# Kernel optimization log

Measured on AMD Instinct MI355X. Metric: run time of the kernel, lower is better.

Reference implementation:

```python
import jax, jax.numpy as jnp
import numpy as np

B, N, M, D, H, DK = 4, 2048, 1024, 512, 8, 64  # H*DK == D (required by residual E + E_)
SCALE = 1.0 / np.sqrt(DK)
NEG = -9e15


def setup_inputs() -> dict:
    key = jax.random.key(0)
    ks = jax.random.split(key, 24)
    def W(k, din, dout):
        return (0.02 * jax.random.truncated_normal(k, -2.0, 2.0, (din, dout))).astype(jnp.float32)
    inp = {
        'X': jax.random.normal(ks[0], (B, N, D), jnp.float32),
        'incidence_matrix': jax.random.randint(ks[1], (B, N, M), 0, 2, jnp.int32),
        'attn_bias': jnp.zeros((1,), jnp.float32),
        'E': jax.random.normal(ks[2], (B, M, D), jnp.float32),
        'Wqn': W(ks[3], D, H * DK), 'bqn': jnp.zeros((H * DK,), jnp.float32),
        'Wkn': W(ks[4], D, H * DK), 'bkn': jnp.zeros((H * DK,), jnp.float32),
        'Wvn': W(ks[5], D, H * DK), 'bvn': jnp.zeros((H * DK,), jnp.float32),
        'Wqe': W(ks[6], D, H * DK), 'bqe': jnp.zeros((H * DK,), jnp.float32),
        'Wke': W(ks[7], D, H * DK), 'bke': jnp.zeros((H * DK,), jnp.float32),
        'Wve': W(ks[8], D, H * DK), 'bve': jnp.zeros((H * DK,), jnp.float32),
        'Wm1': W(ks[9], D, D), 'bm1': jnp.zeros((D,), jnp.float32),
        'Wm2': W(ks[10], D, D), 'bm2': jnp.zeros((D,), jnp.float32),
        'g_ln': jnp.ones((D,), jnp.float32), 'b_ln': jnp.zeros((D,), jnp.float32),
    }
    return inp


def _heads(x, Wt, b):
    # [B, L, D] -> [B, H, L, DK]
    b_, l_ = x.shape[0], x.shape[1]
    return (x @ Wt + b).reshape(b_, l_, H, DK).transpose(0, 2, 1, 3)


def _merge(x):
    # [B, H, L, DK] -> [B, L, H*DK]
    b_, _, l_, _ = x.shape
    return x.transpose(0, 2, 1, 3).reshape(b_, l_, H * DK)


def _layernorm(x, g, b, eps=1e-7):
    mu = jnp.mean(x, axis=-1, keepdims=True)
    var = jnp.var(x, axis=-1, keepdims=True)
    return (x - mu) * jax.lax.rsqrt(var + eps) * g + b


def _gelu(x):
    return jax.nn.gelu(x, approximate=False)


def reference(X, incidence_matrix, attn_bias, E,
              Wqn, bqn, Wkn, bkn, Wvn, bvn,
              Wqe, bqe, Wke, bke, Wve, bve,
              Wm1, bm1, Wm2, bm2, g_ln, b_ln):
    q_n = _heads(X, Wqn, bqn)   # [B,H,N,DK]
    k_n = _heads(X, Wkn, bkn)
    v_n = _heads(X, Wvn, bvn)
    q_e = _heads(E, Wqe, bqe)   # [B,H,M,DK]

    # edge attends over nodes: [B,H,M,N], masked by incidence^T
    att_e = jnp.einsum('bhmd,bhnd->bhmn', q_e, k_n) * SCALE
    mask_e = (incidence_matrix > 0).transpose(0, 2, 1)[:, None, :, :]  # [B,1,M,N]
    att_e = jnp.where(mask_e, att_e, NEG)
    w_e = jax.nn.softmax(att_e, axis=-1)
    E_ = _gelu(jnp.einsum('bhmn,bhnd->bhmd', w_e, v_n))
    E_ = _merge(E_)                                   # [B,M,D]
    E_ = _layernorm(E + E_, g_ln, b_ln)
    E_ = _gelu(E_ @ Wm1 + bm1) @ Wm2 + bm2            # MLP

    k_e = _heads(E_, Wke, bke)  # [B,H,M,DK]
    v_e = _heads(E_, Wve, bve)

    # node attends over edges: [B,H,N,M], masked by incidence
    att_n = jnp.einsum('bhnd,bhmd->bhnm', q_n, k_e) * SCALE
    mask_n = (incidence_matrix > 0)[:, None, :, :]    # [B,1,N,M]
    att_n = jnp.where(mask_n, att_n, NEG)
    w_n = jax.nn.softmax(att_n, axis=-1)
    X_ = _gelu(jnp.einsum('bhnm,bhmd->bhnd', w_n, v_e))
    X_ = _merge(X_)                                   # [B,N,D]
    return (X_, E_)
```

## Files before the change

### kernel.cpp

```cpp
#include <hip/hip_runtime.h>

typedef unsigned short u16;
typedef unsigned int   u32;
typedef unsigned long long u64;

typedef __attribute__((ext_vector_type(8))) short  bf16x8;
typedef __attribute__((ext_vector_type(16))) float f32x16;

#define SC2 0.1803368801111243f
#define CS2 11.541560327111707f

__device__ __forceinline__ float bf2f(u16 h) { return __uint_as_float(((u32)h) << 16); }
__device__ __forceinline__ u16 f2bf(float f) {
  u32 u = __float_as_uint(f);
  return (u16)((u + 0x7FFFu + ((u >> 16) & 1u)) >> 16);
}
__device__ __forceinline__ float gelu_f(float x) {
  return 0.5f * x * (1.0f + erff(x * 0.70710678118654752440f));
}
__device__ __forceinline__ void unpack8(uint4 u, float* d) {
  d[0] = __uint_as_float(u.x << 16); d[1] = __uint_as_float(u.x & 0xffff0000u);
  d[2] = __uint_as_float(u.y << 16); d[3] = __uint_as_float(u.y & 0xffff0000u);
  d[4] = __uint_as_float(u.z << 16); d[5] = __uint_as_float(u.z & 0xffff0000u);
  d[6] = __uint_as_float(u.w << 16); d[7] = __uint_as_float(u.w & 0xffff0000u);
}
__device__ __forceinline__ void dma16(const u16* g, u16* l) {
  __builtin_amdgcn_global_load_lds(
      (const __attribute__((address_space(1))) u32*)g,
      (__attribute__((address_space(3))) u32*)l, 16, 0, 0);
}

__global__ void detect_dtype(const u16* __restrict__ X, u32* __restrict__ flag) {
  int lane = threadIdx.x;
  int bad = 0;
  #pragma unroll
  for (int i = 0; i < 8; ++i) {
    u16 v = X[i * 64 + lane];
    int e = (v >> 7) & 0xFF;
    if (e >= 0x88) bad++;
  }
  #pragma unroll
  for (int o = 1; o < 64; o <<= 1) bad += __shfl_xor(bad, o);
  if (lane == 0) *flag = (bad > 16) ? 1u : 0u;
}

__global__ __launch_bounds__(256) void fill_diag(u32* __restrict__ out, float base,
                                                 const u32* __restrict__ flag) {
  float v = base + (*flag ? 4000.0f : 0.0f);
  u16 h = f2bf(v);
  out[blockIdx.x * 256 + threadIdx.x] = (u32)h | ((u32)h << 16);
}

__global__ __launch_bounds__(256) void conv_bf16(const void* __restrict__ src,
                                                 u16* __restrict__ dst, int n,
                                                 const u32* __restrict__ flag) {
  int i = (blockIdx.x * 256 + threadIdx.x) * 8;
  if (i >= n) return;
  if (*flag) {
    const float* s = (const float*)src + i;
    float4 a = *(const float4*)s;
    float4 b = *(const float4*)(s + 4);
    uint4 o;
    o.x = (u32)f2bf(a.x) | ((u32)f2bf(a.y) << 16);
    o.y = (u32)f2bf(a.z) | ((u32)f2bf(a.w) << 16);
    o.z = (u32)f2bf(b.x) | ((u32)f2bf(b.y) << 16);
    o.w = (u32)f2bf(b.z) | ((u32)f2bf(b.w) << 16);
    *(uint4*)(dst + i) = o;
  } else {
    *(uint4*)(dst + i) = *(const uint4*)((const u16*)src + i);
  }
}

__global__ __launch_bounds__(256) void conv_vec10(
    const void* p0, const void* p1, const void* p2, const void* p3, const void* p4,
    const void* p5, const void* p6, const void* p7, const void* p8, const void* p9,
    u16* __restrict__ dst, const u32* __restrict__ flag) {
  const void* ps[10] = {p0, p1, p2, p3, p4, p5, p6, p7, p8, p9};
  int fl = (int)(*flag);
  for (int idx = threadIdx.x; idx < 5120; idx += 256) {
    int slot = idx >> 9, off = idx & 511;
    u16 v;
    if (fl) v = f2bf(((const float*)ps[slot])[off]);
    else    v = ((const u16*)ps[slot])[off];
    dst[idx] = v;
  }
}

__global__ __launch_bounds__(256) void wtrans(
    const void* w0, const void* w1, const void* w2, const void* w3,
    const void* w4, const void* w5, const void* w6, const void* w7,
    u16* __restrict__ WT, const u32* __restrict__ flag) {
  const void* wsrc[8] = {w0, w1, w2, w3, w4, w5, w6, w7};
  __shared__ u16 tile[32][33];
  int z = blockIdx.z;
  const void* W = wsrc[z];
  u16* Wt = WT + (size_t)z * 262144;
  int fl = (int)(*flag);
  int tx = threadIdx.x & 31, ty = threadIdx.x >> 5;
  int bx = blockIdx.x * 32, by = blockIdx.y * 32;
  #pragma unroll
  for (int i = 0; i < 4; ++i) {
    int r = ty + 8 * i;
    size_t src = (size_t)(by + r) * 512 + bx + tx;
    tile[r][tx] = fl ? f2bf(((const float*)W)[src]) : ((const u16*)W)[src];
  }
  __syncthreads();
  #pragma unroll
  for (int i = 0; i < 4; ++i) {
    int r = ty + 8 * i;
    Wt[(size_t)(bx + r) * 512 + by + tx] = tile[tx][r];
  }
}

__global__ __launch_bounds__(256) void transposeV(const u16* __restrict__ Vp,
                                                  u16* __restrict__ VT, int Lk) {
  __shared__ u16 tile[64][72];
  int t = threadIdx.x;
  int nt = blockIdx.x;
  int bh = blockIdx.y;
  int nw = Lk >> 6;
  const u16* src = Vp + ((size_t)bh * Lk + nt * 64) * 64;
  int key = t >> 2, seg = t & 3;
  int dc0 = seg * 2, dc1 = seg * 2 + 1;
  uint4 a  = *(const uint4*)(src + key * 64 + ((dc0 ^ (key & 7)) << 3));
  uint4 b2 = *(const uint4*)(src + key * 64 + ((dc1 ^ (key & 7)) << 3));
  *(uint4*)&tile[key][dc0 * 8] = a;
  *(uint4*)&tile[key][dc1 * 8] = b2;
  __syncthreads();
  int d = t >> 2;
  u32 wb[8];
  #pragma unroll
  for (int i = 0; i < 8; ++i) {
    u32 lo = tile[seg * 16 + 2 * i][d];
    u32 hi = tile[seg * 16 + 2 * i + 1][d];
    wb[i] = lo | (hi << 16);
  }
  u16* base = VT + (((size_t)bh * nw + nt) * 64 + d) * 64;
  int kc0 = seg * 2, kc1 = seg * 2 + 1;
  uint4 o0; o0.x = wb[0]; o0.y = wb[1]; o0.z = wb[2]; o0.w = wb[3];
  uint4 o1; o1.x = wb[4]; o1.y = wb[5]; o1.z = wb[6]; o1.w = wb[7];
  *(uint4*)(base + ((kc0 ^ (d & 7)) << 3)) = o0;
  *(uint4*)(base + ((kc1 ^ (d & 7)) << 3)) = o1;
}

__global__ __launch_bounds__(256) void pack_rows(const int* __restrict__ inc,
                                                 u64* __restrict__ packNT) {
  int gid  = blockIdx.x * 4 + (threadIdx.x >> 6);
  int lane = threadIdx.x & 63;
  int w  = gid & 15;
  int bn = gid >> 4;
  int b = bn >> 11, n = bn & 2047;
  int v = inc[(size_t)bn * 1024 + (w << 6) + lane];
  u64 mask = __ballot(v > 0);
  if (lane == 0) packNT[((size_t)(b * 16 + w)) * 2048 + n] = mask;
}

__global__ __launch_bounds__(256) void pack_cols(const int* __restrict__ inc,
                                                 u64* __restrict__ packTT) {
  int m = blockIdx.x * 256 + threadIdx.x;
  int w = blockIdx.y;
  int b = blockIdx.z;
  const int* base = inc + ((size_t)b * 2048 + (size_t)w * 64) * 1024 + m;
  u64 out = 0;
  #pragma unroll 8
  for (int j = 0; j < 64; ++j)
    if (base[(size_t)j * 1024] > 0) out |= (1ull << j);
  packTT[((size_t)(b * 32 + w)) * 1024 + m] = out;
}

__global__ __launch_bounds__(256) void gemm_tiled(const u16* __restrict__ A,
                                                  const u16* __restrict__ Wt0, u32 wtStride,
                                                  const u16* __restrict__ bias0, u32 bStride,
                                                  u16* __restrict__ C0, u32 cStride,
                                                  int act, int blocksPerMat,
                                                  u32 modeMask, int lkshift,
                                                  void* __restrict__ out2, size_t out2_off,
                                                  const u32* __restrict__ flag) {
  __shared__ u16 As[2][8192];
  __shared__ u16 Bs[2][8192];
  int mat = blockIdx.x / blocksPerMat;
  int blk = blockIdx.x % blocksPerMat;
  const u16* Wt = Wt0 + (size_t)mat * wtStride;
  const u16* bias = bias0 + (size_t)mat * bStride;
  u16* C = C0 + (size_t)mat * cStride;
  int mode = (modeMask >> mat) & 1u;
  int f32o = out2 ? (int)(*flag) : 0;
  int tm = blk >> 2, tn = blk & 3;
  int m0 = tm * 128, n0 = tn * 128;

  int t = threadIdx.x;
  int wave = t >> 6, lane = t & 63;
  int nl = lane & 31, h32 = lane >> 5;
  int wm = wave >> 1, wn = wave & 1;

  int srow = lane >> 3;
  int gch  = (lane & 7) ^ srow;
  const u16* Ab = A  + ((size_t)m0 + wave * 32) * 512 + (size_t)srow * 512 + gch * 8;
  const u16* Bb = Wt + ((size_t)n0 + wave * 32) * 512 + (size_t)srow * 512 + gch * 8;
  u16* AsW = &As[0][0] + wave * 32 * 64;
  u16* BsW = &Bs[0][0] + wave * 32 * 64;

  #pragma unroll
  for (int c = 0; c < 4; ++c) {
    dma16(Ab + (size_t)c * 8 * 512, AsW + c * 8 * 64);
    dma16(Bb + (size_t)c * 8 * 512, BsW + c * 8 * 64);
  }
  __syncthreads();

  f32x16 a00 = {}, a01 = {}, a10 = {}, a11 = {};

  for (int kk = 0; kk < 8; ++kk) {
    int buf = kk & 1;
    if (kk + 1 < 8) {
      int k0n = (kk + 1) * 64;
      u16* AD = &As[buf ^ 1][0] + wave * 32 * 64;
      u16* BD = &Bs[buf ^ 1][0] + wave * 32 * 64;
      #pragma unroll
      for (int c = 0; c < 4; ++c) {
        dma16(Ab + (size_t)c * 8 * 512 + k0n, AD + c * 8 * 64);
        dma16(Bb + (size_t)c * 8 * 512 + k0n, BD + c * 8 * 64);
      }
    }
    const u16* Ab_s = &As[buf][0];
    const u16* Bb_s = &Bs[buf][0];
    int ar0 = wm * 64 + nl, ar1 = wm * 64 + 32 + nl;
    int br0 = wn * 64 + nl, br1 = wn * 64 + 32 + nl;
    #pragma unroll
    for (int ks = 0; ks < 4; ++ks) {
      int sw = (((ks * 2 + h32) ^ (nl & 7)) << 3);
      bf16x8 fa0 = *(const bf16x8*)(Ab_s + ar0 * 64 + sw);
      bf16x8 fa1 = *(const bf16x8*)(Ab_s + ar1 * 64 + sw);
      bf16x8 fb0 = *(const bf16x8*)(Bb_s + br0 * 64 + sw);
      bf16x8 fb1 = *(const bf16x8*)(Bb_s + br1 * 64 + sw);
      a00 = __builtin_amdgcn_mfma_f32_32x32x16_bf16(fa0, fb0, a00, 0, 0, 0);
      a01 = __builtin_amdgcn_mfma_f32_32x32x16_bf16(fa0, fb1, a01, 0, 0, 0);
      a10 = __builtin_amdgcn_mfma_f32_32x32x16_bf16(fa1, fb0, a10, 0, 0, 0);
      a11 = __builtin_amdgcn_mfma_f32_32x32x16_bf16(fa1, fb1, a11, 0, 0, 0);
    }
    __syncthreads();
  }

  int nw = 1 << (lkshift - 6);
  #pragma unroll
  for (int am = 0; am < 2; ++am) {
    #pragma unroll
    for (int bn = 0; bn < 2; ++bn) {
      const f32x16* accp = am == 0 ? (bn == 0 ? &a00 : &a01)
                                   : (bn == 0 ? &a10 : &a11);
      f32x16 acc = *accp;
      int cn = n0 + wn * 64 + bn * 32 + nl;
      float bv = bf2f(bias[cn]);
      #pragma unroll
      for (int g = 0; g < 16; ++g) {
        int rm = m0 + wm * 64 + am * 32 + (g & 3) + 8 * (g >> 2) + 4 * h32;
        float v = acc[g] + bv;
        if (act) v = gelu_f(v);
        if (mode) {
          int bb = rm >> lkshift;
          int key = rm & ((1 << lkshift) - 1);
          int nt = key >> 6, kl = key & 63;
          int d = cn & 63;
          size_t ad = ((((size_t)bb * 8 + (cn >> 6)) * nw + nt) * 64 + kl) * 64
                      + (((d >> 3) ^ (kl & 7)) << 3) + (d & 7);
          C[ad] = f2bf(v);
        } else {
          size_t ad = (size_t)rm * 512 + cn;
          C[ad] = f2bf(v);
          if (out2) {
            if (f32o) ((float*)out2)[out2_off + ad] = v;
            else      ((u16*)out2)[out2_off + ad] = f2bf(v);
          }
        }
      }
    }
  }
}

__global__ __launch_bounds__(128, 2) void flash_mfma(
    const u16* __restrict__ Q,
    const u16* __restrict__ Kp,
    const u16* __restrict__ VTp,
    const u64* __restrict__ maskT,
    void* __restrict__ Outv,
    u16* __restrict__ Opart, float* __restrict__ Lpart,
    int Lq, int Lk, int splits, int is_final, const u32* __restrict__ flag) {
  __shared__ u16 K_s[2][4096];
  __shared__ u16 V_s[2][4096];
  __shared__ u16 P_s[2][2048];

  int t = threadIdx.x;
  int wave = t >> 6, lane = t & 63;
  int nl = lane & 31, h32 = lane >> 5;
  int qtiles = Lq >> 6;
  int nwords = Lk >> 6;
  int r2 = blockIdx.x % (qtiles * 32);
  int split = blockIdx.x / (qtiles * 32);
  int qt = r2 % qtiles;
  int bh = r2 / qtiles;
  int h = bh & 7, b = bh >> 3;
  int row0 = qt * 64 + wave * 32;
  int per = nwords / splits;
  int tile0 = split * per;
  int f32o = is_final ? (int)(*flag) : 0;

  bf16x8 qf[4];
  {
    const u16* qp = Q + ((size_t)(b * Lq) + row0 + nl) * 512 + h * 64 + h32 * 8;
    #pragma unroll
    for (int ks = 0; ks < 4; ++ks) qf[ks] = *(const bf16x8*)(qp + ks * 16);
  }
  const u16* Kbh = Kp + (size_t)bh * Lk * 64;
  const u16* Vbh = VTp + (size_t)bh * nwords * 4096;
  const u64* mrow = maskT + (size_t)b * nwords * Lq + row0 + nl;

  f32x16 o0 = {}, o1 = {};
  float lsum = 0.f;

  {
    const u16* TK = Kbh + (size_t)tile0 * 4096;
    const u16* TV = Vbh + (size_t)tile0 * 4096;
    #pragma unroll
    for (int c = 0; c < 4; ++c) {
      int ch = c * 2 + wave;
      dma16(TK + ch * 512 + lane * 8, &K_s[0][ch * 512]);
      dma16(TV + ch * 512 + lane * 8, &V_s[0][ch * 512]);
    }
  }
  __syncthreads();

  for (int i = 0; i < per; ++i) {
    int nt = tile0 + i;
    int buf = i & 1;
    if (i + 1 < per) {
      const u16* TK = Kbh + (size_t)(nt + 1) * 4096;
      const u16* TV = Vbh + (size_t)(nt + 1) * 4096;
      u16* KD = K_s[buf ^ 1];
      u16* VD = V_s[buf ^ 1];
      #pragma unroll
      for (int c = 0; c < 4; ++c) {
        int ch = c * 2 + wave;
        dma16(TK + ch * 512 + lane * 8, KD + ch * 512);
        dma16(TV + ch * 512 + lane * 8, VD + ch * 512);
      }
    }
    u64 mymask = mrow[(size_t)nt * Lq];
    u32 mlo = (u32)mymask;
    u32 mhi = (u32)(mymask >> 32);

    f32x16 s0 = {}, s1 = {};
    #pragma unroll
    for (int ks = 0; ks < 4; ++ks) {
      int ch = ks * 2 + h32;
      bf16x8 k0 = *(const bf16x8*)&K_s[buf][nl * 64 + ((ch ^ (nl & 7)) << 3)];
      bf16x8 k1 = *(const bf16x8*)&K_s[buf][(32 + nl) * 64 + ((ch ^ (nl & 7)) << 3)];
      s0 = __builtin_amdgcn_mfma_f32_32x32x16_bf16(k0, qf[ks], s0, 0, 0, 0);
      s1 = __builtin_amdgcn_mfma_f32_32x32x16_bf16(k1, qf[ks], s1, 0, 0, 0);
    }
    #pragma unroll
    for (int gg = 0; gg < 4; ++gg) {
      float pv0[4], pv1[4];
      #pragma unroll
      for (int r = 0; r < 4; ++r) {
        int g = gg * 4 + r;
        int key = r + 8 * gg + 4 * h32;
        float e0 = exp2f(fmaf(s0[g], SC2, -CS2));
        float e1 = exp2f(fmaf(s1[g], SC2, -CS2));
        pv0[r] = ((mlo >> key) & 1u) ? e0 : 0.f;
        pv1[r] = ((mhi >> key) & 1u) ? e1 : 0.f;
        lsum += pv0[r] + pv1[r];
      }
      uint2 a0, a1;
      a0.x = (__float_as_uint(pv0[0]) >> 16) | (__float_as_uint(pv0[1]) & 0xffff0000u);
      a0.y = (__float_as_uint(pv0[2]) >> 16) | (__float_as_uint(pv0[3]) & 0xffff0000u);
      a1.x = (__float_as_uint(pv1[0]) >> 16) | (__float_as_uint(pv1[1]) & 0xffff0000u);
      a1.y = (__float_as_uint(pv1[2]) >> 16) | (__float_as_uint(pv1[3]) & 0xffff0000u);
      *(uint2*)&P_s[wave][gg * 256 + nl * 8 + 4 * h32]       = a0;
      *(uint2*)&P_s[wave][(4 + gg) * 256 + nl * 8 + 4 * h32] = a1;
    }
    asm volatile("s_waitcnt lgkmcnt(0)" ::: "memory");
    #pragma unroll
    for (int ks2 = 0; ks2 < 4; ++ks2) {
      int ch = ks2 * 2 + h32;
      bf16x8 pf = *(const bf16x8*)&P_s[wave][ch * 256 + nl * 8];
      bf16x8 v0 = *(const bf16x8*)&V_s[buf][nl * 64 + ((ch ^ (nl & 7)) << 3)];
      bf16x8 v1 = *(const bf16x8*)&V_s[buf][(32 + nl) * 64 + ((ch ^ (nl & 7)) << 3)];
      o0 = __builtin_amdgcn_mfma_f32_32x32x16_bf16(pf, v0, o0, 0, 0, 0);
      o1 = __builtin_amdgcn_mfma_f32_32x32x16_bf16(pf, v1, o1, 0, 0, 0);
    }
    __syncthreads();
  }
  lsum += __shfl_xor(lsum, 32);

  if (Opart) {
    u16* ob = Opart + (size_t)split * 2097152;
    #pragma unroll
    for (int g = 0; g < 16; ++g) {
      int m = (g & 3) + 8 * (g >> 2) + 4 * h32;
      size_t base = ((size_t)(b * Lq) + row0 + m) * 512 + h * 64;
      ob[base + nl]      = f2bf(o0[g]);
      ob[base + 32 + nl] = f2bf(o1[g]);
    }
    if (h32 == 0)
      Lpart[(size_t)split * 32768 + ((size_t)(b * Lq) + row0 + nl) * 8 + h] = lsum;
  } else {
    #pragma unroll
    for (int g = 0; g < 16; ++g) {
      int m = (g & 3) + 8 * (g >> 2) + 4 * h32;
      float lv = __shfl(lsum, m);
      float inv = 1.0f / (lv + 1e-30f);
      size_t base = ((size_t)(b * Lq) + row0 + m) * 512 + h * 64;
      float v0 = gelu_f(o0[g] * inv);
      float v1 = gelu_f(o1[g] * inv);
      if (f32o) {
        ((float*)Outv)[base + nl]      = v0;
        ((float*)Outv)[base + 32 + nl] = v1;
      } else {
        ((u16*)Outv)[base + nl]      = f2bf(v0);
        ((u16*)Outv)[base + 32 + nl] = f2bf(v1);
      }
    }
  }
}

__global__ __launch_bounds__(256) void ln_fused(const u16* __restrict__ Op,
                                                const float* __restrict__ Lp,
                                                const u16* __restrict__ E,
                                                const u16* __restrict__ g,
                                                const u16* __restrict__ bb,
                                                u16* __restrict__ out) {
  int r = blockIdx.x;
  int t = threadIdx.x;
  int e = t * 2;
  int h = e >> 6;
  float lv = Lp[r * 8 + h] + Lp[32768 + r * 8 + h] + 1e-30f;
  float inv = 1.0f / lv;
  size_t idx = (size_t)r * 512 + e;
  u32 u0 = *(const u32*)&Op[idx];
  u32 u1 = *(const u32*)&Op[2097152 + idx];
  u32 ue = *(const u32*)&E[idx];
  float x0 = bf2f((u16)(ue & 0xffffu)) +
             gelu_f((bf2f((u16)(u0 & 0xffffu)) + bf2f((u16)(u1 & 0xffffu))) * inv);
  float x1 = bf2f((u16)(ue >> 16)) +
             gelu_f((bf2f((u16)(u0 >> 16)) + bf2f((u16)(u1 >> 16))) * inv);
  float s = x0 + x1, q = x0 * x0 + x1 * x1;
  #pragma unroll
  for (int o = 32; o; o >>= 1) { s += __shfl_down(s, o); q += __shfl_down(q, o); }
  __shared__ float red[8];
  int wv = t >> 6, ln = t & 63;
  if (ln == 0) { red[wv] = s; red[4 + wv] = q; }
  __syncthreads();
  s = red[0] + red[1] + red[2] + red[3];
  q = red[4] + red[5] + red[6] + red[7];
  float mean = s * (1.f / 512.f);
  float var  = q * (1.f / 512.f) - mean * mean;
  float rs = rsqrtf(var + 1e-7f);
  u32 ug = *(const u32*)(g + e);
  u32 ub = *(const u32*)(bb + e);
  float y0 = (x0 - mean) * rs * bf2f((u16)(ug & 0xffffu)) + bf2f((u16)(ub & 0xffffu));
  float y1 = (x1 - mean) * rs * bf2f((u16)(ug >> 16)) + bf2f((u16)(ub >> 16));
  *(u32*)(out + idx) = (u32)f2bf(y0) | ((u32)f2bf(y1) << 16);
}

extern "C" void kernel_launch(void* const* d_in, const int* in_sizes, int n_in,
                              void* d_out, int out_size, void* d_ws, size_t ws_size,
                              hipStream_t stream) {
  (void)in_sizes; (void)n_in; (void)out_size;
  const int* inc = (const int*)d_in[1];

  char* ws = (char*)d_ws;
  u32* FLAG = (u32*)ws;
  u16* VEC  = (u16*)(ws + 1024);
  u16* WT   = (u16*)(ws + 65536);
  u16* XB   = (u16*)(ws + 8454144);
  u16* EB   = (u16*)(ws + 16842752);
  u16* QN   = (u16*)(ws + 21037056);
  u16* KN   = (u16*)(ws + 29425664);
  u16* VN   = (u16*)(ws + 37814272);
  u16* QE   = (u16*)(ws + 46202880);
  u16* EATT = (u16*)(ws + 50397184);
  u16* EFIN = (u16*)(ws + 54591488);
  u64* PACKT = (u64*)(ws + 58785792);
  u64* PACKN = (u64*)(ws + 59834368);
  const size_t NEEDED = 60882944;
  u16* ELN = (u16*)(ws + 29425664);
  u16* H1  = (u16*)(ws + 33619968);
  u16* KE  = (u16*)(ws + 37814272);
  u16* Opart = XB;
  float* Lpart = (float*)(ws + 37814272);
  u16* VTn = (u16*)d_out;
  u16* VTe = EATT;
  u16* VE  = (u16*)(ws + 42008576);

  detect_dtype<<<1, 64, 0, stream>>>((const u16*)d_in[0], FLAG);

  if (ws_size < NEEDED) {
    fill_diag<<<8192, 256, 0, stream>>>((u32*)d_out,
                                        1000.0f + (float)(ws_size >> 20), FLAG);
    return;
  }

  conv_bf16<<<2048, 256, 0, stream>>>(d_in[0], XB, 4194304, FLAG);
  conv_bf16<<<1024, 256, 0, stream>>>(d_in[3], EB, 2097152, FLAG);
  conv_vec10<<<1, 256, 0, stream>>>(d_in[5], d_in[7], d_in[9], d_in[11], d_in[13],
                                    d_in[15], d_in[17], d_in[19], d_in[20], d_in[21],
                                    VEC, FLAG);
  wtrans<<<dim3(16, 16, 8), 256, 0, stream>>>(d_in[4], d_in[6], d_in[8], d_in[10],
                                              d_in[12], d_in[14], d_in[16], d_in[18],
                                              WT, FLAG);
  pack_cols<<<dim3(4, 32, 4), 256, 0, stream>>>(inc, PACKT);
  pack_rows<<<32768, 256, 0, stream>>>(inc, PACKN);

  gemm_tiled<<<768, 256, 0, stream>>>(XB, WT, 262144, VEC, 512,
                                      QN, 4194304, 0, 256, 0b110u, 11,
                                      nullptr, 0, FLAG);
  gemm_tiled<<<128, 256, 0, stream>>>(EB, WT + 3 * 262144, 0, VEC + 3 * 512, 0,
                                      QE, 0, 0, 128, 0, 11, nullptr, 0, FLAG);

  transposeV<<<dim3(32, 32), 256, 0, stream>>>(VN, VTn, 2048);

  flash_mfma<<<1024, 128, 0, stream>>>(QE, KN, VTn, PACKT, nullptr,
                                       Opart, Lpart, 1024, 2048, 2, 0, FLAG);

  ln_fused<<<4096, 256, 0, stream>>>(Opart, Lpart, EB,
                                     VEC + 8 * 512, VEC + 9 * 512, ELN);
  gemm_tiled<<<128, 256, 0, stream>>>(ELN, WT + 6 * 262144, 0, VEC + 6 * 512, 0,
                                      H1, 0, 1, 128, 0, 11, nullptr, 0, FLAG);
  gemm_tiled<<<128, 256, 0, stream>>>(H1, WT + 7 * 262144, 0, VEC + 7 * 512, 0,
                                      EFIN, 0, 0, 128, 0, 11,
                                      d_out, 4194304, FLAG);

  gemm_tiled<<<256, 256, 0, stream>>>(EFIN, WT + 4 * 262144, 262144, VEC + 4 * 512, 512,
                                      KE, 2097152, 0, 128, 0b11u, 10,
                                      nullptr, 0, FLAG);
  transposeV<<<dim3(16, 32), 256, 0, stream>>>(VE, VTe, 1024);

  flash_mfma<<<1024, 128, 0, stream>>>(QN, KE, VTe, PACKN, d_out,
                                       nullptr, nullptr, 2048, 1024, 1, 1, FLAG);
}
```

Before: 387.6 us.

## Split attention over more key chunks and keep P in registers via permlane swap

Edge attention now splits its keys into four chunks and node attention into two, each with its own partial-output buffer. A new combine kernel normalizes and applies GELU for the node path, and ln_fused sums four partials for the edge path. Inside flash_mfma, the probability tile is no longer staged through LDS; it is regrouped across the two half-waves with v_permlane32_swap. The change also adds s_setprio around the MFMA loops and raises occupancy to three blocks per CU. The aim is more blocks in flight and less LDS traffic and waiting, at the price of extra partial writes, an extra combine launch and more workspace aliasing.

```diff
diff --git a/kernel.cpp b/kernel.cpp
--- a/kernel.cpp
+++ b/kernel.cpp
@@ -6,6 +6,7 @@
 
 typedef __attribute__((ext_vector_type(8))) short  bf16x8;
 typedef __attribute__((ext_vector_type(16))) float f32x16;
+typedef __attribute__((ext_vector_type(4))) u32    u32x4;
 
 #define SC2 0.1803368801111243f
 #define CS2 11.541560327111707f
@@ -28,6 +29,9 @@
   __builtin_amdgcn_global_load_lds(
       (const __attribute__((address_space(1))) u32*)g,
       (__attribute__((address_space(3))) u32*)l, 16, 0, 0);
+}
+__device__ __forceinline__ void plane32swap(u32& a, u32& b) {
+  asm volatile("v_permlane32_swap_b32 %0, %1" : "+v"(a), "+v"(b));
 }
 
 __global__ void detect_dtype(const u16* __restrict__ X, u32* __restrict__ flag) {
@@ -276,17 +280,16 @@
   }
 }
 
-__global__ __launch_bounds__(128, 2) void flash_mfma(
+__global__ __launch_bounds__(128, 3) void flash_mfma(
     const u16* __restrict__ Q,
     const u16* __restrict__ Kp,
     const u16* __restrict__ VTp,
     const u64* __restrict__ maskT,
-    void* __restrict__ Outv,
-    u16* __restrict__ Opart, float* __restrict__ Lpart,
-    int Lq, int Lk, int splits, int is_final, const u32* __restrict__ flag) {
+    u16* __restrict__ Opart, u16* __restrict__ Opart2,
+    float* __restrict__ Lpart,
+    int Lq, int Lk, int splits, size_t opstride, int lpstride) {
   __shared__ u16 K_s[2][4096];
   __shared__ u16 V_s[2][4096];
-  __shared__ u16 P_s[2][2048];
 
   int t = threadIdx.x;
   int wave = t >> 6, lane = t & 63;
@@ -301,7 +304,6 @@
   int row0 = qt * 64 + wave * 32;
   int per = nwords / splits;
   int tile0 = split * per;
-  int f32o = is_final ? (int)(*flag) : 0;
 
   bf16x8 qf[4];
   {
@@ -348,6 +350,7 @@
     u32 mhi = (u32)(mymask >> 32);
 
     f32x16 s0 = {}, s1 = {};
+    __builtin_amdgcn_s_setprio(1);
     #pragma unroll
     for (int ks = 0; ks < 4; ++ks) {
       int ch = ks * 2 + h32;
@@ -356,6 +359,9 @@
       s0 = __builtin_amdgcn_mfma_f32_32x32x16_bf16(k0, qf[ks], s0, 0, 0, 0);
       s1 = __builtin_amdgcn_mfma_f32_32x32x16_bf16(k1, qf[ks], s1, 0, 0, 0);
     }
+    __builtin_amdgcn_s_setprio(0);
+
+    u32 pk0[4][2], pk1[4][2];
     #pragma unroll
     for (int gg = 0; gg < 4; ++gg) {
       float pv0[4], pv1[4];
@@ -369,60 +375,50 @@
         pv1[r] = ((mhi >> key) & 1u) ? e1 : 0.f;
         lsum += pv0[r] + pv1[r];
       }
-      uint2 a0, a1;
-      a0.x = (__float_as_uint(pv0[0]) >> 16) | (__float_as_uint(pv0[1]) & 0xffff0000u);
-      a0.y = (__float_as_uint(pv0[2]) >> 16) | (__float_as_uint(pv0[3]) & 0xffff0000u);
-      a1.x = (__float_as_uint(pv1[0]) >> 16) | (__float_as_uint(pv1[1]) & 0xffff0000u);
-      a1.y = (__float_as_uint(pv1[2]) >> 16) | (__float_as_uint(pv1[3]) & 0xffff0000u);
-      *(uint2*)&P_s[wave][gg * 256 + nl * 8 + 4 * h32]       = a0;
-      *(uint2*)&P_s[wave][(4 + gg) * 256 + nl * 8 + 4 * h32] = a1;
-    }
-    asm volatile("s_waitcnt lgkmcnt(0)" ::: "memory");
+      pk0[gg][0] = (__float_as_uint(pv0[0]) >> 16) | (__float_as_uint(pv0[1]) & 0xffff0000u);
+      pk0[gg][1] = (__float_as_uint(pv0[2]) >> 16) | (__float_as_uint(pv0[3]) & 0xffff0000u);
+      pk1[gg][0] = (__float_as_uint(pv1[0]) >> 16) | (__float_as_uint(pv1[1]) & 0xffff0000u);
+      pk1[gg][1] = (__float_as_uint(pv1[2]) >> 16) | (__float_as_uint(pv1[3]) & 0xffff0000u);
+    }
+
+    __builtin_amdgcn_s_setprio(1);
     #pragma unroll
     for (int ks2 = 0; ks2 < 4; ++ks2) {
+      int g0 = (ks2 & 1) * 2;
+      u32 f0 = (ks2 < 2) ? pk0[g0][0]     : pk1[g0][0];
+      u32 f1 = (ks2 < 2) ? pk0[g0][1]     : pk1[g0][1];
+      u32 f2 = (ks2 < 2) ? pk0[g0 + 1][0] : pk1[g0 + 1][0];
+      u32 f3 = (ks2 < 2) ? pk0[g0 + 1][1] : pk1[g0 + 1][1];
+      plane32swap(f0, f2);
+      plane32swap(f1, f3);
+      u32x4 fw; fw.x = f0; fw.y = f1; fw.z = f2; fw.w = f3;
+      bf16x8 pf = __builtin_bit_cast(bf16x8, fw);
       int ch = ks2 * 2 + h32;
-      bf16x8 pf = *(const bf16x8*)&P_s[wave][ch * 256 + nl * 8];
       bf16x8 v0 = *(const bf16x8*)&V_s[buf][nl * 64 + ((ch ^ (nl & 7)) << 3)];
       bf16x8 v1 = *(const bf16x8*)&V_s[buf][(32 + nl) * 64 + ((ch ^ (nl & 7)) << 3)];
       o0 = __builtin_amdgcn_mfma_f32_32x32x16_bf16(pf, v0, o0, 0, 0, 0);
       o1 = __builtin_amdgcn_mfma_f32_32x32x16_bf16(pf, v1, o1, 0, 0, 0);
     }
+    __builtin_amdgcn_s_setprio(0);
     __syncthreads();
   }
   lsum += __shfl_xor(lsum, 32);
 
-  if (Opart) {
-    u16* ob = Opart + (size_t)split * 2097152;
-    #pragma unroll
-    for (int g = 0; g < 16; ++g) {
-      int m = (g & 3) + 8 * (g >> 2) + 4 * h32;
-      size_t base = ((size_t)(b * Lq) + row0 + m) * 512 + h * 64;
-      ob[base + nl]      = f2bf(o0[g]);
-      ob[base + 32 + nl] = f2bf(o1[g]);
-    }
-    if (h32 == 0)
-      Lpart[(size_t)split * 32768 + ((size_t)(b * Lq) + row0 + nl) * 8 + h] = lsum;
-  } else {
-    #pragma unroll
-    for (int g = 0; g < 16; ++g) {
-      int m = (g & 3) + 8 * (g >> 2) + 4 * h32;
-      float lv = __shfl(lsum, m);
-      float inv = 1.0f / (lv + 1e-30f);
-      size_t base = ((size_t)(b * Lq) + row0 + m) * 512 + h * 64;
-      float v0 = gelu_f(o0[g] * inv);
-      float v1 = gelu_f(o1[g] * inv);
-      if (f32o) {
-        ((float*)Outv)[base + nl]      = v0;
-        ((float*)Outv)[base + 32 + nl] = v1;
-      } else {
-        ((u16*)Outv)[base + nl]      = f2bf(v0);
-        ((u16*)Outv)[base + 32 + nl] = f2bf(v1);
-      }
-    }
-  }
+  u16* ob = (split >= 2) ? Opart2 + (size_t)(split - 2) * opstride
+                         : Opart  + (size_t)split * opstride;
+  #pragma unroll
+  for (int g = 0; g < 16; ++g) {
+    int m = (g & 3) + 8 * (g >> 2) + 4 * h32;
+    size_t base = ((size_t)(b * Lq) + row0 + m) * 512 + h * 64;
+    ob[base + nl]      = f2bf(o0[g]);
+    ob[base + 32 + nl] = f2bf(o1[g]);
+  }
+  if (h32 == 0)
+    Lpart[(size_t)split * lpstride + ((size_t)(b * Lq) + row0 + nl) * 8 + h] = lsum;
 }
 
 __global__ __launch_bounds__(256) void ln_fused(const u16* __restrict__ Op,
+                                                const u16* __restrict__ Op2,
                                                 const float* __restrict__ Lp,
                                                 const u16* __restrict__ E,
                                                 const u16* __restrict__ g,
@@ -432,16 +428,22 @@
   int t = threadIdx.x;
   int e = t * 2;
   int h = e >> 6;
-  float lv = Lp[r * 8 + h] + Lp[32768 + r * 8 + h] + 1e-30f;
+  float lv = 1e-30f;
+  #pragma unroll
+  for (int s = 0; s < 4; ++s) lv += Lp[s * 32768 + r * 8 + h];
   float inv = 1.0f / lv;
   size_t idx = (size_t)r * 512 + e;
   u32 u0 = *(const u32*)&Op[idx];
   u32 u1 = *(const u32*)&Op[2097152 + idx];
+  u32 u2 = *(const u32*)&Op2[idx];
+  u32 u3 = *(const u32*)&Op2[2097152 + idx];
   u32 ue = *(const u32*)&E[idx];
-  float x0 = bf2f((u16)(ue & 0xffffu)) +
-             gelu_f((bf2f((u16)(u0 & 0xffffu)) + bf2f((u16)(u1 & 0xffffu))) * inv);
-  float x1 = bf2f((u16)(ue >> 16)) +
-             gelu_f((bf2f((u16)(u0 >> 16)) + bf2f((u16)(u1 >> 16))) * inv);
+  float a0 = bf2f((u16)(u0 & 0xffffu)) + bf2f((u16)(u1 & 0xffffu)) +
+             bf2f((u16)(u2 & 0xffffu)) + bf2f((u16)(u3 & 0xffffu));
+  float a1 = bf2f((u16)(u0 >> 16)) + bf2f((u16)(u1 >> 16)) +
+             bf2f((u16)(u2 >> 16)) + bf2f((u16)(u3 >> 16));
+  float x0 = bf2f((u16)(ue & 0xffffu)) + gelu_f(a0 * inv);
+  float x1 = bf2f((u16)(ue >> 16)) + gelu_f(a1 * inv);
   float s = x0 + x1, q = x0 * x0 + x1 * x1;
   #pragma unroll
   for (int o = 32; o; o >>= 1) { s += __shfl_down(s, o); q += __shfl_down(q, o); }
@@ -459,6 +461,29 @@
   float y0 = (x0 - mean) * rs * bf2f((u16)(ug & 0xffffu)) + bf2f((u16)(ub & 0xffffu));
   float y1 = (x1 - mean) * rs * bf2f((u16)(ug >> 16)) + bf2f((u16)(ub >> 16));
   *(u32*)(out + idx) = (u32)f2bf(y0) | ((u32)f2bf(y1) << 16);
+}
+
+__global__ __launch_bounds__(256) void combine_node(const u16* __restrict__ Op,
+                                                    const float* __restrict__ Lp,
+                                                    void* __restrict__ out,
+                                                    const u32* __restrict__ flag) {
+  int r = blockIdx.x;
+  int t = threadIdx.x;
+  int e = t * 2;
+  int h = e >> 6;
+  float lv = Lp[r * 8 + h] + Lp[65536 + r * 8 + h] + 1e-30f;
+  float inv = 1.0f / lv;
+  size_t idx = (size_t)r * 512 + e;
+  u32 u0 = *(const u32*)&Op[idx];
+  u32 u1 = *(const u32*)&Op[10485760 + idx];
+  float x0 = gelu_f((bf2f((u16)(u0 & 0xffffu)) + bf2f((u16)(u1 & 0xffffu))) * inv);
+  float x1 = gelu_f((bf2f((u16)(u0 >> 16)) + bf2f((u16)(u1 >> 16))) * inv);
+  if (*flag) {
+    float2 o; o.x = x0; o.y = x1;
+    *(float2*)&((float*)out)[idx] = o;
+  } else {
+    *(u32*)((u16*)out + idx) = (u32)f2bf(x0) | ((u32)f2bf(x1) << 16);
+  }
 }
 
 extern "C" void kernel_launch(void* const* d_in, const int* in_sizes, int n_in,
@@ -485,8 +510,6 @@
   u16* ELN = (u16*)(ws + 29425664);
   u16* H1  = (u16*)(ws + 33619968);
   u16* KE  = (u16*)(ws + 37814272);
-  u16* Opart = XB;
-  float* Lpart = (float*)(ws + 37814272);
   u16* VTn = (u16*)d_out;
   u16* VTe = EATT;
   u16* VE  = (u16*)(ws + 42008576);
@@ -518,11 +541,16 @@
 
   transposeV<<<dim3(32, 32), 256, 0, stream>>>(VN, VTn, 2048);
 
-  flash_mfma<<<1024, 128, 0, stream>>>(QE, KN, VTn, PACKT, nullptr,
-                                       Opart, Lpart, 1024, 2048, 2, 0, FLAG);
-
-  ln_fused<<<4096, 256, 0, stream>>>(Opart, Lpart, EB,
-                                     VEC + 8 * 512, VEC + 9 * 512, ELN);
+  {
+    u16* OpartE  = XB;
+    u16* OpartE2 = (u16*)(ws + 37814272);
+    float* LpartE = (float*)(ws + 54591488);
+    flash_mfma<<<2048, 128, 0, stream>>>(QE, KN, VTn, PACKT,
+                                         OpartE, OpartE2, LpartE,
+                                         1024, 2048, 4, 2097152, 32768);
+    ln_fused<<<4096, 256, 0, stream>>>(OpartE, OpartE2, LpartE, EB,
+                                       VEC + 8 * 512, VEC + 9 * 512, ELN);
+  }
   gemm_tiled<<<128, 256, 0, stream>>>(ELN, WT + 6 * 262144, 0, VEC + 6 * 512, 0,
                                       H1, 0, 1, 128, 0, 11, nullptr, 0, FLAG);
   gemm_tiled<<<128, 256, 0, stream>>>(H1, WT + 7 * 262144, 0, VEC + 7 * 512, 0,
@@ -534,6 +562,12 @@
                                       nullptr, 0, FLAG);
   transposeV<<<dim3(16, 32), 256, 0, stream>>>(VE, VTe, 1024);
 
-  flash_mfma<<<1024, 128, 0, stream>>>(QN, KE, VTe, PACKN, d_out,
-                                       nullptr, nullptr, 2048, 1024, 1, 1, FLAG);
-}
+  {
+    u16* OpartN = XB;
+    float* LpartN = (float*)(ws + 16842752);
+    flash_mfma<<<2048, 128, 0, stream>>>(QN, KE, VTe, PACKN,
+                                         OpartN, OpartN , LpartN,
+                                         2048, 1024, 2, 10485760, 65536);
+    combine_node<<<8192, 256, 0, stream>>>(OpartN, LpartN, d_out, FLAG);
+  }
+}
```

Result: slower. 400.9 us (+3.4%).

## Pass softmax probabilities between MFMAs via permlane32 swap instead of LDS

Applied to the files above, without the earlier changes.

Keeps the packed bf16 probability fragments in registers and rearranges them into the B-operand layout with v_permlane32_swap. This drops the LDS round trip, the waitcnt on it, and the per-wave P_s buffer. It also prefetches the next tile's mask word one iteration ahead so the global load latency overlaps compute. The cost is some extra register pressure, and correctness now depends on the lane-swap mapping matching the old LDS layout.

```diff
diff --git a/kernel.cpp b/kernel.cpp
--- a/kernel.cpp
+++ b/kernel.cpp
@@ -6,6 +6,7 @@
 
 typedef __attribute__((ext_vector_type(8))) short  bf16x8;
 typedef __attribute__((ext_vector_type(16))) float f32x16;
+typedef __attribute__((ext_vector_type(4))) u32    u32x4;
 
 #define SC2 0.1803368801111243f
 #define CS2 11.541560327111707f
@@ -18,16 +19,13 @@
 __device__ __forceinline__ float gelu_f(float x) {
   return 0.5f * x * (1.0f + erff(x * 0.70710678118654752440f));
 }
-__device__ __forceinline__ void unpack8(uint4 u, float* d) {
-  d[0] = __uint_as_float(u.x << 16); d[1] = __uint_as_float(u.x & 0xffff0000u);
-  d[2] = __uint_as_float(u.y << 16); d[3] = __uint_as_float(u.y & 0xffff0000u);
-  d[4] = __uint_as_float(u.z << 16); d[5] = __uint_as_float(u.z & 0xffff0000u);
-  d[6] = __uint_as_float(u.w << 16); d[7] = __uint_as_float(u.w & 0xffff0000u);
-}
 __device__ __forceinline__ void dma16(const u16* g, u16* l) {
   __builtin_amdgcn_global_load_lds(
       (const __attribute__((address_space(1))) u32*)g,
       (__attribute__((address_space(3))) u32*)l, 16, 0, 0);
+}
+__device__ __forceinline__ void plane32swap(u32& a, u32& b) {
+  asm("v_permlane32_swap_b32 %0, %1" : "+v"(a), "+v"(b));
 }
 
 __global__ void detect_dtype(const u16* __restrict__ X, u32* __restrict__ flag) {
@@ -286,7 +284,6 @@
     int Lq, int Lk, int splits, int is_final, const u32* __restrict__ flag) {
   __shared__ u16 K_s[2][4096];
   __shared__ u16 V_s[2][4096];
-  __shared__ u16 P_s[2][2048];
 
   int t = threadIdx.x;
   int wave = t >> 6, lane = t & 63;
@@ -326,6 +323,7 @@
       dma16(TV + ch * 512 + lane * 8, &V_s[0][ch * 512]);
     }
   }
+  u64 nextmask = mrow[(size_t)tile0 * Lq];
   __syncthreads();
 
   for (int i = 0; i < per; ++i) {
@@ -343,7 +341,8 @@
         dma16(TV + ch * 512 + lane * 8, VD + ch * 512);
       }
     }
-    u64 mymask = mrow[(size_t)nt * Lq];
+    u64 mymask = nextmask;
+    if (i + 1 < per) nextmask = mrow[(size_t)(nt + 1) * Lq];
     u32 mlo = (u32)mymask;
     u32 mhi = (u32)(mymask >> 32);
 
@@ -356,6 +355,8 @@
       s0 = __builtin_amdgcn_mfma_f32_32x32x16_bf16(k0, qf[ks], s0, 0, 0, 0);
       s1 = __builtin_amdgcn_mfma_f32_32x32x16_bf16(k1, qf[ks], s1, 0, 0, 0);
     }
+
+    u32 pk0[4][2], pk1[4][2];
     #pragma unroll
     for (int gg = 0; gg < 4; ++gg) {
       float pv0[4], pv1[4];
@@ -369,19 +370,24 @@
         pv1[r] = ((mhi >> key) & 1u) ? e1 : 0.f;
         lsum += pv0[r] + pv1[r];
       }
-      uint2 a0, a1;
-      a0.x = (__float_as_uint(pv0[0]) >> 16) | (__float_as_uint(pv0[1]) & 0xffff0000u);
-      a0.y = (__float_as_uint(pv0[2]) >> 16) | (__float_as_uint(pv0[3]) & 0xffff0000u);
-      a1.x = (__float_as_uint(pv1[0]) >> 16) | (__float_as_uint(pv1[1]) & 0xffff0000u);
-      a1.y = (__float_as_uint(pv1[2]) >> 16) | (__float_as_uint(pv1[3]) & 0xffff0000u);
-      *(uint2*)&P_s[wave][gg * 256 + nl * 8 + 4 * h32]       = a0;
-      *(uint2*)&P_s[wave][(4 + gg) * 256 + nl * 8 + 4 * h32] = a1;
-    }
-    asm volatile("s_waitcnt lgkmcnt(0)" ::: "memory");
+      pk0[gg][0] = (__float_as_uint(pv0[0]) >> 16) | (__float_as_uint(pv0[1]) & 0xffff0000u);
+      pk0[gg][1] = (__float_as_uint(pv0[2]) >> 16) | (__float_as_uint(pv0[3]) & 0xffff0000u);
+      pk1[gg][0] = (__float_as_uint(pv1[0]) >> 16) | (__float_as_uint(pv1[1]) & 0xffff0000u);
+      pk1[gg][1] = (__float_as_uint(pv1[2]) >> 16) | (__float_as_uint(pv1[3]) & 0xffff0000u);
+    }
+
     #pragma unroll
     for (int ks2 = 0; ks2 < 4; ++ks2) {
+      int g0 = (ks2 & 1) * 2;
+      u32 f0 = (ks2 < 2) ? pk0[g0][0]     : pk1[g0][0];
+      u32 f1 = (ks2 < 2) ? pk0[g0][1]     : pk1[g0][1];
+      u32 f2 = (ks2 < 2) ? pk0[g0 + 1][0] : pk1[g0 + 1][0];
+      u32 f3 = (ks2 < 2) ? pk0[g0 + 1][1] : pk1[g0 + 1][1];
+      plane32swap(f0, f2);
+      plane32swap(f1, f3);
+      u32x4 fw; fw.x = f0; fw.y = f1; fw.z = f2; fw.w = f3;
+      bf16x8 pf = __builtin_bit_cast(bf16x8, fw);
       int ch = ks2 * 2 + h32;
-      bf16x8 pf = *(const bf16x8*)&P_s[wave][ch * 256 + nl * 8];
       bf16x8 v0 = *(const bf16x8*)&V_s[buf][nl * 64 + ((ch ^ (nl & 7)) << 3)];
       bf16x8 v1 = *(const bf16x8*)&V_s[buf][(32 + nl) * 64 + ((ch ^ (nl & 7)) << 3)];
       o0 = __builtin_amdgcn_mfma_f32_32x32x16_bf16(pf, v0, o0, 0, 0, 0);
```

Result: slower. 397.6 us (+2.6%).
